# Kernel tuning notes

Measured on AMD Instinct MI355X. Metric: run time of the kernel, lower is better.

The kernel has to match this reference:

```python
import jax, jax.numpy as jnp
import numpy as np

BLOCK = 32           # sparsity_config.block
STRIDE_BLOCKS = 4    # stride 128 // block 32
B, H, L, HD = 2, 16, 4096, 64


def _make_fixed_layout(nb, bs):
    """DeepSpeed 'fixed' unidirectional layout, numverts=vertsize=1 (same for all heads)."""
    lay = np.zeros((nb, nb), dtype=np.int64)
    # local: lower-triangular within each stride window
    for i in range(0, nb, bs):
        for j in range(i, i + bs):
            lay[j, i:j + 1] = 1
    # global: vertical stripe at column offset bs-1 of every window, causal (col < row)
    start = bs - 1
    for i in range(nb):
        for j in range(start, i, bs):
            lay[i, j] = 1
    rows, cols = np.nonzero(lay)  # sorted by row
    return jnp.asarray(rows, jnp.int32), jnp.asarray(cols, jnp.int32)


def setup_inputs() -> dict:
    key = jax.random.key(0)
    kq, kk, kv = jax.random.split(key, 3)
    query = jax.random.normal(kq, (B, H, L, HD), jnp.float32)
    key_t = jax.random.normal(kk, (B, H, L, HD), jnp.float32)
    value = jax.random.normal(kv, (B, H, L, HD), jnp.float32)
    rows, cols = _make_fixed_layout(L // BLOCK, STRIDE_BLOCKS)
    return {"query": query, "key": key_t, "value": value,
            "rows": rows, "cols": cols, "block": BLOCK}


def reference(query, key, value, rows, cols, block):
    b, h, l, hd = query.shape
    nb = l // block
    scale = float(hd) ** (-0.5)
    # [nb, B, H, block, hd] with block-row axis leading for gather/scatter
    qb = jnp.moveaxis(query.reshape(b, h, nb, block, hd), 2, 0)
    kb = jnp.moveaxis(key.reshape(b, h, nb, block, hd), 2, 0)
    vb = jnp.moveaxis(value.reshape(b, h, nb, block, hd), 2, 0)
    # sdd: scores only on active blocks -> [nnz, B, H, block, block]
    s = jnp.einsum('nbhqd,nbhkd->nbhqk', qb[rows], kb[cols]) * scale
    # block-sparse softmax over each query row (segment reduce over blocks sharing a row)
    m_blk = s.max(-1)  # [nnz, B, H, block]
    row_max = jnp.full((nb, b, h, block), -jnp.inf, s.dtype).at[rows].max(m_blk)
    e = jnp.exp(s - row_max[rows][..., None])
    denom = jnp.zeros((nb, b, h, block), s.dtype).at[rows].add(e.sum(-1))
    p = e / denom[rows][..., None]
    # dsd: probs @ value, scatter-add into block rows
    ob = jnp.zeros((nb, b, h, block, hd), s.dtype).at[rows].add(
        jnp.einsum('nbhqk,nbhkd->nbhqd', p, vb[cols]))
    return jnp.moveaxis(ob, 0, 2).reshape(b, h, l, hd)
```

## Files before the change

kernel.cpp:

```cpp
#include <hip/hip_runtime.h>
#include <math.h>

#define BH    32
#define LSEQ  4096
#define HD    64
#define BLK   32
#define NB    128
#define NWIN  32
#define QSCALE 0.18033688011112042f

#define KSTR 34
#define VSTR 17

typedef _Float16 h2  __attribute__((ext_vector_type(2)));
typedef _Float16 h8  __attribute__((ext_vector_type(8)));
typedef float    f16v __attribute__((ext_vector_type(16)));

static __device__ __forceinline__ h2 pk(float a, float b) {
    return __builtin_bit_cast(h2, __builtin_amdgcn_cvt_pkrtz(a, b));
}
static __device__ __forceinline__ unsigned pku(float a, float b) {
    return __builtin_bit_cast(unsigned, __builtin_amdgcn_cvt_pkrtz(a, b));
}
static __device__ __forceinline__ short h16(float x) {
    return __builtin_bit_cast(short, (_Float16)x);
}
static __device__ __forceinline__ h8 mk8(h2 a, h2 b, h2 c, h2 d) {
    h8 r;
    r[0] = a[0]; r[1] = a[1]; r[2] = b[0]; r[3] = b[1];
    r[4] = c[0]; r[5] = c[1]; r[6] = d[0]; r[7] = d[1];
    return r;
}

__global__ __launch_bounds__(256)
void sparse_attn_win(const float* __restrict__ Q, const float* __restrict__ K,
                     const float* __restrict__ V, float* __restrict__ out)
{
    const int w    = NWIN - 1 - (int)blockIdx.x;
    const int bh   = (int)blockIdx.y;
    const int t    = (int)threadIdx.x;
    const int d    = t >> 6;
    const int lane = t & 63;
    const int l31  = lane & 31;
    const int h    = lane >> 5;
    const int r    = 4 * w + d;

    __shared__ __align__(16) unsigned kbuf[2][BLK * KSTR];
    __shared__ __align__(16) unsigned vbuf[2][HD * VSTR];

    const size_t base = (size_t)bh * (LSEQ * HD);

    const float* qp = Q + base + (size_t)(r * BLK + l31) * HD + 8 * h;
    h8 qf[4];
#pragma unroll
    for (int tt = 0; tt < 4; ++tt) {
        float4 a = *(const float4*)(qp + 16 * tt);
        float4 b = *(const float4*)(qp + 16 * tt + 4);
        qf[tt] = mk8(pk(a.x * QSCALE, a.y * QSCALE), pk(a.z * QSCALE, a.w * QSCALE),
                     pk(b.x * QSCALE, b.y * QSCALE), pk(b.z * QSCALE, b.w * QSCALE));
    }

    f16v o0 = {}, o1 = {};
    float lsum = 0.0f;

    const int n    = w + 4;
    const int srow = t >> 3;
    const int sdg  = t & 7;

    auto stagef = [&](int j, int b) {
        const int c = (j < w) ? (4 * j + 3) : (4 * w + (j - w));
        const float* kg = K + base + (size_t)(c * BLK + srow) * HD + sdg * 8;
        float4 a  = *(const float4*)kg;
        float4 bb = *(const float4*)(kg + 4);
        uint2 w0, w1;
        w0.x = pku(a.x, a.y);   w0.y = pku(a.z, a.w);
        w1.x = pku(bb.x, bb.y); w1.y = pku(bb.z, bb.w);
        *(uint2*)&kbuf[b][srow * KSTR + sdg * 4]     = w0;
        *(uint2*)&kbuf[b][srow * KSTR + sdg * 4 + 2] = w1;

        const float* vg = V + base + (size_t)(c * BLK + srow) * HD + sdg * 8;
        float4 va = *(const float4*)vg;
        float4 vb2 = *(const float4*)(vg + 4);
        short* vs = (short*)&vbuf[b][0];
        const int vd0 = sdg * 8;
        vs[(vd0 + 0) * (2 * VSTR) + srow] = h16(va.x);
        vs[(vd0 + 1) * (2 * VSTR) + srow] = h16(va.y);
        vs[(vd0 + 2) * (2 * VSTR) + srow] = h16(va.z);
        vs[(vd0 + 3) * (2 * VSTR) + srow] = h16(va.w);
        vs[(vd0 + 4) * (2 * VSTR) + srow] = h16(vb2.x);
        vs[(vd0 + 5) * (2 * VSTR) + srow] = h16(vb2.y);
        vs[(vd0 + 6) * (2 * VSTR) + srow] = h16(vb2.z);
        vs[(vd0 + 7) * (2 * VSTR) + srow] = h16(vb2.w);
    };

    stagef(0, 0);

    for (int j = 0; j < n; ++j) {
        __syncthreads();
        if (j + 1 < n) stagef(j + 1, (j + 1) & 1);

        if (j < w || (j - w) <= d) {
            const unsigned* kb = kbuf[j & 1];
            const unsigned* vb = vbuf[j & 1];

            f16v st = {};
#pragma unroll
            for (int tt = 0; tt < 4; ++tt) {
                const int kw = l31 * KSTR + 8 * tt + 4 * h;
                uint2 u0 = *(const uint2*)&kb[kw];
                uint2 u1 = *(const uint2*)&kb[kw + 2];
                uint4 uu; uu.x = u0.x; uu.y = u0.y; uu.z = u1.x; uu.w = u1.y;
                h8 kf = __builtin_bit_cast(h8, uu);
                st = __builtin_amdgcn_mfma_f32_32x32x16_f16(kf, qf[tt], st, 0, 0, 0);
            }

            float ps[16];
#pragma unroll
            for (int g = 0; g < 16; ++g) { ps[g] = __builtin_exp2f(st[g]); lsum += ps[g]; }
            h2 ph[8];
#pragma unroll
            for (int jj = 0; jj < 8; ++jj) ph[jj] = pk(ps[2 * jj], ps[2 * jj + 1]);

#pragma unroll
            for (int t2 = 0; t2 < 2; ++t2) {
                h2 s0 = h ? ph[4 * t2]     : ph[4 * t2 + 2];
                h2 s1 = h ? ph[4 * t2 + 1] : ph[4 * t2 + 3];
                int i0 = __shfl_xor(__builtin_bit_cast(int, s0), 32);
                int i1 = __shfl_xor(__builtin_bit_cast(int, s1), 32);
                h2 g0 = __builtin_bit_cast(h2, i0), g1 = __builtin_bit_cast(h2, i1);
                h2 c0 = h ? g0 : ph[4 * t2];
                h2 c1 = h ? g1 : ph[4 * t2 + 1];
                h2 c2 = h ? ph[4 * t2 + 2] : g0;
                h2 c3 = h ? ph[4 * t2 + 3] : g1;
                h8 pa = mk8(c0, c1, c2, c3);

                const int va0 = l31 * VSTR + 8 * t2 + 4 * h;
                const int va1 = (32 + l31) * VSTR + 8 * t2 + 4 * h;
                uint4 u0, u1;
                u0.x = vb[va0]; u0.y = vb[va0 + 1]; u0.z = vb[va0 + 2]; u0.w = vb[va0 + 3];
                u1.x = vb[va1]; u1.y = vb[va1 + 1]; u1.z = vb[va1 + 2]; u1.w = vb[va1 + 3];
                h8 vf0 = __builtin_bit_cast(h8, u0);
                h8 vf1 = __builtin_bit_cast(h8, u1);
                o0 = __builtin_amdgcn_mfma_f32_32x32x16_f16(pa, vf0, o0, 0, 0, 0);
                o1 = __builtin_amdgcn_mfma_f32_32x32x16_f16(pa, vf1, o1, 0, 0, 0);
            }
        }
    }

    lsum += __shfl_xor(lsum, 32);
    const float inv = 1.0f / lsum;

    float* op = out + base + (size_t)(r * BLK) * HD;
#pragma unroll
    for (int g = 0; g < 16; ++g) {
        const int qrow = (g & 3) + 8 * (g >> 2) + 4 * h;
        int iv = __builtin_amdgcn_ds_bpermute(qrow << 2, __float_as_int(inv));
        const float invq = __int_as_float(iv);
        op[(size_t)qrow * HD + l31]      = o0[g] * invq;
        op[(size_t)qrow * HD + 32 + l31] = o1[g] * invq;
    }
}

extern "C" void kernel_launch(void* const* d_in, const int* in_sizes, int n_in,
                              void* d_out, int out_size, void* d_ws, size_t ws_size,
                              hipStream_t stream) {
    const float* Q = (const float*)d_in[0];
    const float* K = (const float*)d_in[1];
    const float* V = (const float*)d_in[2];

    dim3 grid(NWIN, BH);
    dim3 block(256);
    sparse_attn_win<<<grid, block, 0, stream>>>(Q, K, V, (float*)d_out);
}
```

Before: 191.7 us.

## Prefetch next K/V block into registers across the loop and widen V LDS reads

Staging is split into a global load of the next block into registers and an LDS write of the current block, issued before the barrier. This lets the global load latency overlap with the MFMA compute instead of stalling inside the staging step. VSTR becomes 18 so the V rows are 8-byte aligned and can be read with uint2 loads instead of scalar ones, at a possible change in LDS bank conflicts. The row-sum accumulation is also split into two independent chains to shorten the dependency.

```diff
diff --git a/kernel.cpp b/kernel.cpp
--- a/kernel.cpp
+++ b/kernel.cpp
@@ -10,7 +10,7 @@
 #define QSCALE 0.18033688011112042f
 
 #define KSTR 34
-#define VSTR 17
+#define VSTR 18
 
 typedef _Float16 h2  __attribute__((ext_vector_type(2)));
 typedef _Float16 h8  __attribute__((ext_vector_type(8)));
@@ -33,8 +33,8 @@
 }
 
 __global__ __launch_bounds__(256)
-void sparse_attn_win(const float* __restrict__ Q, const float* __restrict__ K,
-                     const float* __restrict__ V, float* __restrict__ out)
+void sparse_attn_win2(const float* __restrict__ Q, const float* __restrict__ K,
+                      const float* __restrict__ V, float* __restrict__ out)
 {
     const int w    = NWIN - 1 - (int)blockIdx.x;
     const int bh   = (int)blockIdx.y;
@@ -61,43 +61,50 @@
     }
 
     f16v o0 = {}, o1 = {};
-    float lsum = 0.0f;
+    float2 ls2 = make_float2(0.0f, 0.0f);
 
     const int n    = w + 4;
     const int srow = t >> 3;
     const int sdg  = t & 7;
 
-    auto stagef = [&](int j, int b) {
-        const int c = (j < w) ? (4 * j + 3) : (4 * w + (j - w));
-        const float* kg = K + base + (size_t)(c * BLK + srow) * HD + sdg * 8;
-        float4 a  = *(const float4*)kg;
-        float4 bb = *(const float4*)(kg + 4);
+    const float* kgb = K + base + (size_t)srow * HD + sdg * 8;
+    const float* vgb = V + base + (size_t)srow * HD + sdg * 8;
+
+    float4 kA, kB, vA, vB;
+
+    auto colOf = [&](int j) { return (j < w) ? (4 * j + 3) : (4 * w + (j - w)); };
+
+    auto loadR = [&](int j) {
+        const size_t off = (size_t)colOf(j) * (BLK * HD);
+        kA = *(const float4*)(kgb + off);
+        kB = *(const float4*)(kgb + off + 4);
+        vA = *(const float4*)(vgb + off);
+        vB = *(const float4*)(vgb + off + 4);
+    };
+    auto writeL = [&](int b) {
         uint2 w0, w1;
-        w0.x = pku(a.x, a.y);   w0.y = pku(a.z, a.w);
-        w1.x = pku(bb.x, bb.y); w1.y = pku(bb.z, bb.w);
+        w0.x = pku(kA.x, kA.y); w0.y = pku(kA.z, kA.w);
+        w1.x = pku(kB.x, kB.y); w1.y = pku(kB.z, kB.w);
         *(uint2*)&kbuf[b][srow * KSTR + sdg * 4]     = w0;
         *(uint2*)&kbuf[b][srow * KSTR + sdg * 4 + 2] = w1;
-
-        const float* vg = V + base + (size_t)(c * BLK + srow) * HD + sdg * 8;
-        float4 va = *(const float4*)vg;
-        float4 vb2 = *(const float4*)(vg + 4);
         short* vs = (short*)&vbuf[b][0];
         const int vd0 = sdg * 8;
-        vs[(vd0 + 0) * (2 * VSTR) + srow] = h16(va.x);
-        vs[(vd0 + 1) * (2 * VSTR) + srow] = h16(va.y);
-        vs[(vd0 + 2) * (2 * VSTR) + srow] = h16(va.z);
-        vs[(vd0 + 3) * (2 * VSTR) + srow] = h16(va.w);
-        vs[(vd0 + 4) * (2 * VSTR) + srow] = h16(vb2.x);
-        vs[(vd0 + 5) * (2 * VSTR) + srow] = h16(vb2.y);
-        vs[(vd0 + 6) * (2 * VSTR) + srow] = h16(vb2.z);
-        vs[(vd0 + 7) * (2 * VSTR) + srow] = h16(vb2.w);
+        vs[(vd0 + 0) * (2 * VSTR) + srow] = h16(vA.x);
+        vs[(vd0 + 1) * (2 * VSTR) + srow] = h16(vA.y);
+        vs[(vd0 + 2) * (2 * VSTR) + srow] = h16(vA.z);
+        vs[(vd0 + 3) * (2 * VSTR) + srow] = h16(vA.w);
+        vs[(vd0 + 4) * (2 * VSTR) + srow] = h16(vB.x);
+        vs[(vd0 + 5) * (2 * VSTR) + srow] = h16(vB.y);
+        vs[(vd0 + 6) * (2 * VSTR) + srow] = h16(vB.z);
+        vs[(vd0 + 7) * (2 * VSTR) + srow] = h16(vB.w);
     };
 
-    stagef(0, 0);
+    loadR(0);
 
     for (int j = 0; j < n; ++j) {
+        writeL(j & 1);
+        if (j + 1 < n) loadR(j + 1);
         __syncthreads();
-        if (j + 1 < n) stagef(j + 1, (j + 1) & 1);
 
         if (j < w || (j - w) <= d) {
             const unsigned* kb = kbuf[j & 1];
@@ -116,7 +123,12 @@
 
             float ps[16];
 #pragma unroll
-            for (int g = 0; g < 16; ++g) { ps[g] = __builtin_exp2f(st[g]); lsum += ps[g]; }
+            for (int g = 0; g < 16; ++g) ps[g] = __builtin_exp2f(st[g]);
+#pragma unroll
+            for (int g = 0; g < 8; ++g) {
+                ls2.x += ps[2 * g];
+                ls2.y += ps[2 * g + 1];
+            }
             h2 ph[8];
 #pragma unroll
             for (int jj = 0; jj < 8; ++jj) ph[jj] = pk(ps[2 * jj], ps[2 * jj + 1]);
@@ -136,9 +148,12 @@
 
                 const int va0 = l31 * VSTR + 8 * t2 + 4 * h;
                 const int va1 = (32 + l31) * VSTR + 8 * t2 + 4 * h;
-                uint4 u0, u1;
-                u0.x = vb[va0]; u0.y = vb[va0 + 1]; u0.z = vb[va0 + 2]; u0.w = vb[va0 + 3];
-                u1.x = vb[va1]; u1.y = vb[va1 + 1]; u1.z = vb[va1 + 2]; u1.w = vb[va1 + 3];
+                uint2 x0 = *(const uint2*)&vb[va0];
+                uint2 x1 = *(const uint2*)&vb[va0 + 2];
+                uint2 y0 = *(const uint2*)&vb[va1];
+                uint2 y1 = *(const uint2*)&vb[va1 + 2];
+                uint4 u0; u0.x = x0.x; u0.y = x0.y; u0.z = x1.x; u0.w = x1.y;
+                uint4 u1; u1.x = y0.x; u1.y = y0.y; u1.z = y1.x; u1.w = y1.y;
                 h8 vf0 = __builtin_bit_cast(h8, u0);
                 h8 vf1 = __builtin_bit_cast(h8, u1);
                 o0 = __builtin_amdgcn_mfma_f32_32x32x16_f16(pa, vf0, o0, 0, 0, 0);
@@ -147,6 +162,7 @@
         }
     }
 
+    float lsum = ls2.x + ls2.y;
     lsum += __shfl_xor(lsum, 32);
     const float inv = 1.0f / lsum;
 
@@ -170,5 +186,5 @@
 
     dim3 grid(NWIN, BH);
     dim3 block(256);
-    sparse_attn_win<<<grid, block, 0, stream>>>(Q, K, V, (float*)d_out);
+    sparse_attn_win2<<<grid, block, 0, stream>>>(Q, K, V, (float*)d_out);
 }
```

Result: slower. 215.2 us (+12.2%).
